# Kernel tuning notes

Hardware: AMD Instinct MI355X
Metric: run time of the kernel (lower is better)

The kernel has to match this reference:

```python
import jax, jax.numpy as jnp
import numpy as np

EMB = 1024
HEADS = 16
HEAD_DIM = EMB // HEADS


def setup_inputs() -> dict:
    key = jax.random.key(0)
    ks = jax.random.split(key, 5)
    x = jax.random.normal(ks[0], (2, 2048, EMB), dtype=jnp.float32)
    # per-head projection params, stacked over heads: [H, E, D]
    Wq = jax.random.normal(ks[1], (HEADS, EMB, HEAD_DIM), dtype=jnp.float32)
    Wk = jax.random.normal(ks[2], (HEADS, EMB, HEAD_DIM), dtype=jnp.float32)
    Wv = jax.random.normal(ks[3], (HEADS, EMB, HEAD_DIM), dtype=jnp.float32)
    # output projection (torch Linear weight [out, in], bias=False)
    Wo = jax.random.normal(ks[4], (EMB, EMB), dtype=jnp.float32) * (1.0 / np.sqrt(EMB))
    return {"x": x, "Wq": Wq, "Wk": Wk, "Wv": Wv, "Wo": Wo}


def reference(x, Wq, Wk, Wv, Wo):
    B, T, E = x.shape
    # per-head projections: [B, H, T, D]
    q = jnp.einsum('bte,hed->bhtd', x, Wq)
    k = jnp.einsum('bte,hed->bhtd', x, Wk)
    v = jnp.einsum('bte,hed->bhtd', x, Wv)
    scale = 1.0 / jnp.sqrt(jnp.asarray(HEAD_DIM, dtype=x.dtype))
    scores = jnp.einsum('bhtd,bhsd->bhts', q, k) * scale  # [B,H,T,T]
    s = jax.nn.softmax(scores, axis=-1)
    out = jnp.einsum('bhts,bhsd->bhtd', s, v)
    # concat heads along last dim in head order: [B, T, H*D]
    combined = jnp.transpose(out, (0, 2, 1, 3)).reshape(B, T, E)
    # residual + output projection (Linear bias=False: y = combined @ Wo.T)
    return x + combined @ Wo.T
```

## Files before the change

kernel.cpp:

```cpp
#include <hip/hip_runtime.h>

#define EMB   1024
#define HEADS 16
#define HDIM  64
#define BATCH 2
#define SEQ   2048
#define MROWS (BATCH*SEQ)
#define STR   40
#define QSCALE 0.1803368801111204f

typedef __attribute__((ext_vector_type(8))) short bf16x8;
typedef __attribute__((ext_vector_type(4))) float f32x4;
typedef unsigned short u16;

__device__ __forceinline__ u16 f2bf(float f) {
    unsigned u = __float_as_uint(f);
    u += 0x7fffu + ((u >> 16) & 1u);
    return (u16)(u >> 16);
}
__device__ __forceinline__ float bf2f(u16 h) {
    return __uint_as_float((unsigned)h << 16);
}
__device__ __forceinline__ float fast_exp2(float x) {
#if __has_builtin(__builtin_amdgcn_exp2f)
    return __builtin_amdgcn_exp2f(x);
#else
    return __expf(x * 0.6931471805599453f);
#endif
}
__device__ __forceinline__ unsigned pk_trunc(float lo, float hi) {
    return __builtin_amdgcn_perm(__float_as_uint(hi), __float_as_uint(lo),
                                 0x07060302u);
}

#define SWZ(r, ch) ((((r) << 6)) + ((((ch) ^ ((r) & 7))) << 3))

__global__ __launch_bounds__(256)
void prep1(const float* __restrict__ X, const float* __restrict__ Wq,
           const float* __restrict__ Wk,
           u16* __restrict__ Xh, u16* __restrict__ Xl,
           u16* __restrict__ Qth, u16* __restrict__ Qtl,
           u16* __restrict__ Kth, u16* __restrict__ Ktl)
{
    const int bx = blockIdx.x;
    if (bx < 2048) {
        int i = (bx * 256 + threadIdx.x) * 8;
#pragma unroll
        for (int half = 0; half < 2; ++half) {
            float4 v = *(const float4*)(X + i + half * 4);
            ushort4 hi, lo;
            hi.x = f2bf(v.x); lo.x = f2bf(v.x - bf2f(hi.x));
            hi.y = f2bf(v.y); lo.y = f2bf(v.y - bf2f(hi.y));
            hi.z = f2bf(v.z); lo.z = f2bf(v.z - bf2f(hi.z));
            hi.w = f2bf(v.w); lo.w = f2bf(v.w - bf2f(hi.w));
            *(ushort4*)(Xh + i + half * 4) = hi;
            *(ushort4*)(Xl + i + half * 4) = lo;
        }
    } else {
        const int f = bx - 2048;
        const int z = f >> 9, y = (f >> 5) & 15, x = f & 31;
        const float* W  = z ? Wk  : Wq;
        u16* Oh         = z ? Kth : Qth;
        u16* Ol         = z ? Ktl : Qtl;
        const int d  = threadIdx.x & 63;
        const int e0 = (x * 4 + (threadIdx.x >> 6)) * 8;
        const float* src = W + ((size_t)y * EMB + e0) * HDIM + d;
        ushort4 h0, h1, l0, l1;
        float v; u16 hv;
        v = src[0 * 64]; hv = f2bf(v); h0.x = hv; l0.x = f2bf(v - bf2f(hv));
        v = src[1 * 64]; hv = f2bf(v); h0.y = hv; l0.y = f2bf(v - bf2f(hv));
        v = src[2 * 64]; hv = f2bf(v); h0.z = hv; l0.z = f2bf(v - bf2f(hv));
        v = src[3 * 64]; hv = f2bf(v); h0.w = hv; l0.w = f2bf(v - bf2f(hv));
        v = src[4 * 64]; hv = f2bf(v); h1.x = hv; l1.x = f2bf(v - bf2f(hv));
        v = src[5 * 64]; hv = f2bf(v); h1.y = hv; l1.y = f2bf(v - bf2f(hv));
        v = src[6 * 64]; hv = f2bf(v); h1.z = hv; l1.z = f2bf(v - bf2f(hv));
        v = src[7 * 64]; hv = f2bf(v); h1.w = hv; l1.w = f2bf(v - bf2f(hv));
        size_t obase = ((size_t)y * HDIM + d) * EMB + e0;
        *(ushort4*)(Oh + obase)     = h0;
        *(ushort4*)(Oh + obase + 4) = h1;
        *(ushort4*)(Ol + obase)     = l0;
        *(ushort4*)(Ol + obase + 4) = l1;
    }
}

__global__ __launch_bounds__(256)
void prep2(const float* __restrict__ Wv, const float* __restrict__ Wo,
           u16* __restrict__ Vth, u16* __restrict__ Woh)
{
    const int f = blockIdx.x;
    if (f < 512) {
        const int y = f >> 5, x = f & 31;
        const int d  = threadIdx.x & 63;
        const int e0 = (x * 4 + (threadIdx.x >> 6)) * 8;
        const float* src = Wv + ((size_t)y * EMB + e0) * HDIM + d;
        ushort4 h0, h1;
        h0.x = f2bf(src[0 * 64]); h0.y = f2bf(src[1 * 64]);
        h0.z = f2bf(src[2 * 64]); h0.w = f2bf(src[3 * 64]);
        h1.x = f2bf(src[4 * 64]); h1.y = f2bf(src[5 * 64]);
        h1.z = f2bf(src[6 * 64]); h1.w = f2bf(src[7 * 64]);
        size_t obase = ((size_t)y * HDIM + d) * EMB + e0;
        *(ushort4*)(Vth + obase)     = h0;
        *(ushort4*)(Vth + obase + 4) = h1;
    } else {
        int i = ((f - 512) * 256 + threadIdx.x) * 8;
#pragma unroll
        for (int half = 0; half < 2; ++half) {
            float4 v = *(const float4*)(Wo + i + half * 4);
            ushort4 o;
            o.x = f2bf(v.x); o.y = f2bf(v.y); o.z = f2bf(v.z); o.w = f2bf(v.w);
            *(ushort4*)(Woh + i + half * 4) = o;
        }
    }
}

__global__ __launch_bounds__(256, 2)
void qkv_z01(const u16* __restrict__ Xh, const u16* __restrict__ Xl,
             const u16* __restrict__ Wqh, const u16* __restrict__ Wql,
             const u16* __restrict__ Wkh, const u16* __restrict__ Wkl,
             u16* __restrict__ Qh, u16* __restrict__ Ql,
             u16* __restrict__ Kh, u16* __restrict__ Kl)
{
    const int z  = blockIdx.z;
    const int m0 = blockIdx.x * 128;
    const int n0 = blockIdx.y * 128;
    const int t    = threadIdx.x;
    const int wave = t >> 6, lane = t & 63;
    const int wm = wave & 1, wn = wave >> 1;
    const int l16 = lane & 15, quad = lane >> 4;

    __shared__ u16 Ahs[128][STR];
    __shared__ u16 Als[128][STR];
    __shared__ u16 Bhs[128][STR];
    __shared__ u16 Bls[128][STR];

    const u16* Bh_g = z ? Wkh : Wqh;
    const u16* Bl_g = z ? Wkl : Wql;

    const int ar0 = t >> 2, ak = (t & 3) * 8, ar1 = ar0 + 64;

    f32x4 acc[4][4];
#pragma unroll
    for (int i = 0; i < 4; ++i)
#pragma unroll
        for (int j = 0; j < 4; ++j) acc[i][j] = (f32x4){0.f, 0.f, 0.f, 0.f};

    bf16x8 cur[8], nxt[8], nx2[8];
#define QK_LOAD(dst, kk)                                                        \
    do {                                                                        \
        dst[0] = *(const bf16x8*)(Xh  + (size_t)(m0 + ar0) * EMB + (kk) + ak);  \
        dst[1] = *(const bf16x8*)(Xh  + (size_t)(m0 + ar1) * EMB + (kk) + ak);  \
        dst[2] = *(const bf16x8*)(Xl  + (size_t)(m0 + ar0) * EMB + (kk) + ak);  \
        dst[3] = *(const bf16x8*)(Xl  + (size_t)(m0 + ar1) * EMB + (kk) + ak);  \
        dst[4] = *(const bf16x8*)(Bh_g + (size_t)(n0 + ar0) * EMB + (kk) + ak); \
        dst[5] = *(const bf16x8*)(Bh_g + (size_t)(n0 + ar1) * EMB + (kk) + ak); \
        dst[6] = *(const bf16x8*)(Bl_g + (size_t)(n0 + ar0) * EMB + (kk) + ak); \
        dst[7] = *(const bf16x8*)(Bl_g + (size_t)(n0 + ar1) * EMB + (kk) + ak); \
    } while (0)

    QK_LOAD(cur, 0);
    QK_LOAD(nxt, 32);

    for (int k0 = 0; k0 < EMB; k0 += 32) {
        __syncthreads();
        *(bf16x8*)&Ahs[ar0][ak] = cur[0];  *(bf16x8*)&Ahs[ar1][ak] = cur[1];
        *(bf16x8*)&Als[ar0][ak] = cur[2];  *(bf16x8*)&Als[ar1][ak] = cur[3];
        *(bf16x8*)&Bhs[ar0][ak] = cur[4];  *(bf16x8*)&Bhs[ar1][ak] = cur[5];
        *(bf16x8*)&Bls[ar0][ak] = cur[6];  *(bf16x8*)&Bls[ar1][ak] = cur[7];
        __syncthreads();

        const int kn = (k0 + 64 < EMB) ? k0 + 64 : 0;
        QK_LOAD(nx2, kn);

        bf16x8 B4h[4], B4l[4];
#pragma unroll
        for (int j = 0; j < 4; ++j) {
            B4h[j] = *(const bf16x8*)&Bhs[wn * 64 + 16 * j + l16][quad * 8];
            B4l[j] = *(const bf16x8*)&Bls[wn * 64 + 16 * j + l16][quad * 8];
        }
#pragma unroll
        for (int i = 0; i < 4; ++i) {
            bf16x8 Ai_h = *(const bf16x8*)&Ahs[wm * 64 + 16 * i + l16][quad * 8];
            bf16x8 Ai_l = *(const bf16x8*)&Als[wm * 64 + 16 * i + l16][quad * 8];
#pragma unroll
            for (int j = 0; j < 4; ++j) {
                acc[i][j] = __builtin_amdgcn_mfma_f32_16x16x32_bf16(Ai_h, B4h[j], acc[i][j], 0, 0, 0);
                acc[i][j] = __builtin_amdgcn_mfma_f32_16x16x32_bf16(Ai_h, B4l[j], acc[i][j], 0, 0, 0);
                acc[i][j] = __builtin_amdgcn_mfma_f32_16x16x32_bf16(Ai_l, B4h[j], acc[i][j], 0, 0, 0);
            }
        }
#pragma unroll
        for (int q = 0; q < 8; ++q) { cur[q] = nxt[q]; nxt[q] = nx2[q]; }
    }
#undef QK_LOAD

    const int b = m0 >> 11;
    const int h = (n0 + wn * 64) >> 6;
    u16* Oh = z ? Kh : Qh;
    u16* Ol = z ? Kl : Ql;
    const float esc = z ? 1.0f : QSCALE;
#pragma unroll
    for (int i = 0; i < 4; ++i)
#pragma unroll
        for (int r = 0; r < 4; ++r) {
            int tt = (m0 & (SEQ - 1)) + wm * 64 + 16 * i + quad * 4 + r;
            size_t rowbase = ((size_t)(b * HEADS + h) * SEQ + tt) * HDIM;
#pragma unroll
            for (int j = 0; j < 4; ++j) {
                int d = 16 * j + l16;
                float v = acc[i][j][r] * esc;
                u16 hv = f2bf(v);
                Oh[rowbase + d] = hv;
                Ol[rowbase + d] = f2bf(v - bf2f(hv));
            }
        }
}

__global__ __launch_bounds__(256, 2)
void qkv_v(const u16* __restrict__ Xh, const u16* __restrict__ Wvt,
           u16* __restrict__ Vt)
{
    const int m0 = blockIdx.x * 128;
    const int n0 = blockIdx.y * 128;
    const int t    = threadIdx.x;
    const int wave = t >> 6, lane = t & 63;
    const int wm = wave & 1, wn = wave >> 1;
    const int l16 = lane & 15, quad = lane >> 4;

    __shared__ u16 Ahs[128][STR];
    __shared__ u16 Bhs[128][STR];

    const int ar0 = t >> 2, ak = (t & 3) * 8, ar1 = ar0 + 64;

    f32x4 acc[4][4];
#pragma unroll
    for (int i = 0; i < 4; ++i)
#pragma unroll
        for (int j = 0; j < 4; ++j) acc[i][j] = (f32x4){0.f, 0.f, 0.f, 0.f};

    bf16x8 cur[4], nxt[4], nx2[4];
#define V_LOAD(dst, kk)                                                         \
    do {                                                                        \
        dst[0] = *(const bf16x8*)(Xh  + (size_t)(m0 + ar0) * EMB + (kk) + ak);  \
        dst[1] = *(const bf16x8*)(Xh  + (size_t)(m0 + ar1) * EMB + (kk) + ak);  \
        dst[2] = *(const bf16x8*)(Wvt + (size_t)(n0 + ar0) * EMB + (kk) + ak);  \
        dst[3] = *(const bf16x8*)(Wvt + (size_t)(n0 + ar1) * EMB + (kk) + ak);  \
    } while (0)

    V_LOAD(cur, 0);
    V_LOAD(nxt, 32);

    for (int k0 = 0; k0 < EMB; k0 += 32) {
        __syncthreads();
        *(bf16x8*)&Ahs[ar0][ak] = cur[0];  *(bf16x8*)&Ahs[ar1][ak] = cur[1];
        *(bf16x8*)&Bhs[ar0][ak] = cur[2];  *(bf16x8*)&Bhs[ar1][ak] = cur[3];
        __syncthreads();

        const int kn = (k0 + 64 < EMB) ? k0 + 64 : 0;
        V_LOAD(nx2, kn);

        bf16x8 B4[4];
#pragma unroll
        for (int j = 0; j < 4; ++j)
            B4[j] = *(const bf16x8*)&Bhs[wn * 64 + 16 * j + l16][quad * 8];
#pragma unroll
        for (int i = 0; i < 4; ++i) {
            bf16x8 Ai = *(const bf16x8*)&Ahs[wm * 64 + 16 * i + l16][quad * 8];
#pragma unroll
            for (int j = 0; j < 4; ++j)
                acc[i][j] = __builtin_amdgcn_mfma_f32_16x16x32_bf16(Ai, B4[j], acc[i][j], 0, 0, 0);
        }
#pragma unroll
        for (int q = 0; q < 4; ++q) { cur[q] = nxt[q]; nxt[q] = nx2[q]; }
    }
#undef V_LOAD

    const int b = m0 >> 11;
    const int h = (n0 + wn * 64) >> 6;
#pragma unroll
    for (int i = 0; i < 4; ++i)
#pragma unroll
        for (int j = 0; j < 4; ++j) {
            int d  = 16 * j + l16;
            int tt = (m0 & (SEQ - 1)) + wm * 64 + 16 * i + quad * 4;
            ushort4 o;
            o.x = f2bf(acc[i][j][0]); o.y = f2bf(acc[i][j][1]);
            o.z = f2bf(acc[i][j][2]); o.w = f2bf(acc[i][j][3]);
            *(ushort4*)(Vt + ((size_t)(b * HEADS + h) * HDIM + d) * SEQ + tt) = o;
        }
}

__global__ __launch_bounds__(256, 2)
void attn_mfma(const u16* __restrict__ Qh, const u16* __restrict__ Ql,
               const u16* __restrict__ Kh, const u16* __restrict__ Kl,
               const u16* __restrict__ Vt, u16* __restrict__ Cb)
{
    const int qt0  = blockIdx.x * 128;
    const int bh   = blockIdx.y;
    const int t    = threadIdx.x;
    const int wave = t >> 6;
    const int lane = t & 63;
    const int l16  = lane & 15;
    const int quad = lane >> 4;

    __shared__ u16 Ksh[4096];
    __shared__ u16 Ksl[4096];
    __shared__ u16 Vs [4096];
    __shared__ u16 Ps [8192];

    const size_t bh_off = (size_t)bh * SEQ * HDIM;
    const u16* Qhb = Qh + bh_off;
    const u16* Qlb = Ql + bh_off;
    const u16* Khb = Kh + bh_off;
    const u16* Klb = Kl + bh_off;
    const u16* Vtb = Vt + bh_off;

    bf16x8 aQh[2][2], aQl[2][2];
#pragma unroll
    for (int g = 0; g < 2; ++g) {
        const int qrow = qt0 + g * 64 + wave * 16 + l16;
        const u16* bH = Qhb + (size_t)qrow * HDIM + quad * 8;
        const u16* bL = Qlb + (size_t)qrow * HDIM + quad * 8;
        aQh[g][0] = *(const bf16x8*)(bH);
        aQh[g][1] = *(const bf16x8*)(bH + 32);
        aQl[g][0] = *(const bf16x8*)(bL);
        aQl[g][1] = *(const bf16x8*)(bL + 32);
    }

    f32x4 accO[2][4];
    float m_i[2] = {-1e30f, -1e30f}, l_i[2] = {0.f, 0.f};
#pragma unroll
    for (int g = 0; g < 2; ++g)
#pragma unroll
        for (int j = 0; j < 4; ++j) accO[g][j] = (f32x4){0.f, 0.f, 0.f, 0.f};

    const int sr0 = t >> 3, sch = t & 7, sr1 = sr0 + 32;
    const int gc  = sch * 8;
    const int so0 = SWZ(sr0, sch), so1 = SWZ(sr1, sch);

    bf16x8 cur[6], nxt[6];
#define KV_LOAD(dst, ss)                                                       \
    do {                                                                       \
        dst[0] = *(const bf16x8*)(Khb + (size_t)((ss) + sr0) * HDIM + gc);     \
        dst[1] = *(const bf16x8*)(Khb + (size_t)((ss) + sr1) * HDIM + gc);     \
        dst[2] = *(const bf16x8*)(Klb + (size_t)((ss) + sr0) * HDIM + gc);     \
        dst[3] = *(const bf16x8*)(Klb + (size_t)((ss) + sr1) * HDIM + gc);     \
        dst[4] = *(const bf16x8*)(Vtb + (size_t)sr0 * SEQ + (ss) + gc);        \
        dst[5] = *(const bf16x8*)(Vtb + (size_t)sr1 * SEQ + (ss) + gc);        \
    } while (0)

    KV_LOAD(cur, 0);

    for (int s0 = 0; s0 < SEQ; s0 += 64) {
        __syncthreads();
        *(bf16x8*)&Ksh[so0] = cur[0];  *(bf16x8*)&Ksh[so1] = cur[1];
        *(bf16x8*)&Ksl[so0] = cur[2];  *(bf16x8*)&Ksl[so1] = cur[3];
        *(bf16x8*)&Vs [so0] = cur[4];  *(bf16x8*)&Vs [so1] = cur[5];
        __syncthreads();

        const int sn = (s0 + 64 < SEQ) ? s0 + 64 : 0;
        KV_LOAD(nxt, sn);

        f32x4 accS[2][4];
#pragma unroll
        for (int g = 0; g < 2; ++g)
#pragma unroll
            for (int i = 0; i < 4; ++i) accS[g][i] = (f32x4){0.f, 0.f, 0.f, 0.f};
#pragma unroll
        for (int c = 0; c < 2; ++c) {
#pragma unroll
            for (int i = 0; i < 4; ++i) {
                bf16x8 kh_ = *(const bf16x8*)&Ksh[SWZ(16 * i + l16, 4 * c + quad)];
                bf16x8 kl_ = *(const bf16x8*)&Ksl[SWZ(16 * i + l16, 4 * c + quad)];
                accS[0][i] = __builtin_amdgcn_mfma_f32_16x16x32_bf16(kh_, aQh[0][c], accS[0][i], 0, 0, 0);
                accS[0][i] = __builtin_amdgcn_mfma_f32_16x16x32_bf16(kl_, aQh[0][c], accS[0][i], 0, 0, 0);
                accS[0][i] = __builtin_amdgcn_mfma_f32_16x16x32_bf16(kh_, aQl[0][c], accS[0][i], 0, 0, 0);
                accS[1][i] = __builtin_amdgcn_mfma_f32_16x16x32_bf16(kh_, aQh[1][c], accS[1][i], 0, 0, 0);
                accS[1][i] = __builtin_amdgcn_mfma_f32_16x16x32_bf16(kl_, aQh[1][c], accS[1][i], 0, 0, 0);
                accS[1][i] = __builtin_amdgcn_mfma_f32_16x16x32_bf16(kh_, aQl[1][c], accS[1][i], 0, 0, 0);
            }
        }

#pragma unroll
        for (int g = 0; g < 2; ++g) {
            float vmax = fmaxf(fmaxf(accS[g][0][0], accS[g][0][1]),
                               fmaxf(accS[g][0][2], accS[g][0][3]));
#pragma unroll
            for (int i = 1; i < 4; ++i)
                vmax = fmaxf(vmax, fmaxf(fmaxf(accS[g][i][0], accS[g][i][1]),
                                         fmaxf(accS[g][i][2], accS[g][i][3])));
            vmax = fmaxf(vmax, __shfl_xor(vmax, 16, 64));
            vmax = fmaxf(vmax, __shfl_xor(vmax, 32, 64));
            float mn   = fmaxf(m_i[g], vmax);
            float alph = fast_exp2(m_i[g] - mn);
            m_i[g] = mn;
            float P[4][4], s = 0.f;
#pragma unroll
            for (int i = 0; i < 4; ++i)
#pragma unroll
                for (int r = 0; r < 4; ++r) {
                    P[i][r] = fast_exp2(accS[g][i][r] - mn);
                    s += P[i][r];
                }
            s += __shfl_xor(s, 16, 64);
            s += __shfl_xor(s, 32, 64);
            l_i[g] = l_i[g] * alph + s;
#pragma unroll
            for (int j = 0; j < 4; ++j) accO[g][j] *= alph;

            const int prow = g * 64 + wave * 16 + l16;
#pragma unroll
            for (int i = 0; i < 4; ++i) {
                uint2 pv;
                pv.x = pk_trunc(P[i][0], P[i][1]);
                pv.y = pk_trunc(P[i][2], P[i][3]);
                *(uint2*)&Ps[SWZ(prow, 2 * i + (quad >> 1)) + ((quad & 1) << 2)] = pv;
            }
        }

#pragma unroll
        for (int c = 0; c < 2; ++c) {
            bf16x8 bP0 = *(const bf16x8*)&Ps[SWZ(wave * 16 + l16,      4 * c + quad)];
            bf16x8 bP1 = *(const bf16x8*)&Ps[SWZ(64 + wave * 16 + l16, 4 * c + quad)];
#pragma unroll
            for (int j = 0; j < 4; ++j) {
                bf16x8 aV = *(const bf16x8*)&Vs[SWZ(16 * j + l16, 4 * c + quad)];
                accO[0][j] = __builtin_amdgcn_mfma_f32_16x16x32_bf16(aV, bP0, accO[0][j], 0, 0, 0);
                accO[1][j] = __builtin_amdgcn_mfma_f32_16x16x32_bf16(aV, bP1, accO[1][j], 0, 0, 0);
            }
        }
#pragma unroll
        for (int q = 0; q < 6; ++q) cur[q] = nxt[q];
    }
#undef KV_LOAD

    const int b = bh >> 4, h = bh & 15;
#pragma unroll
    for (int g = 0; g < 2; ++g) {
        const int row = qt0 + g * 64 + wave * 16 + l16;
        const float inv = 1.f / l_i[g];
#pragma unroll
        for (int j = 0; j < 4; ++j) {
            ushort4 o;
            o.x = f2bf(accO[g][j][0] * inv); o.y = f2bf(accO[g][j][1] * inv);
            o.z = f2bf(accO[g][j][2] * inv); o.w = f2bf(accO[g][j][3] * inv);
            *(ushort4*)&Cb[((size_t)b * SEQ + row) * EMB + h * HDIM + 16 * j + quad * 4] = o;
        }
    }
}

__global__ __launch_bounds__(256, 2)
void oproj_mfma(const u16* __restrict__ Cb, const u16* __restrict__ Woh,
                const float* __restrict__ X, float* __restrict__ Y)
{
    const int m0 = blockIdx.x * 128;
    const int n0 = blockIdx.y * 128;
    const int t    = threadIdx.x;
    const int wave = t >> 6, lane = t & 63;
    const int wm = wave & 1, wn = wave >> 1;
    const int l16 = lane & 15, quad = lane >> 4;

    __shared__ u16 Ahs[128][STR];
    __shared__ u16 Bhs[128][STR];

    const int ar0 = t >> 2, ak = (t & 3) * 8, ar1 = ar0 + 64;

    f32x4 acc[4][4];
#pragma unroll
    for (int i = 0; i < 4; ++i)
#pragma unroll
        for (int j = 0; j < 4; ++j) acc[i][j] = (f32x4){0.f, 0.f, 0.f, 0.f};

    bf16x8 cur[4], nxt[4], nx2[4];
#define O_LOAD(dst, kk)                                                         \
    do {                                                                        \
        dst[0] = *(const bf16x8*)(Cb  + (size_t)(m0 + ar0) * EMB + (kk) + ak);  \
        dst[1] = *(const bf16x8*)(Cb  + (size_t)(m0 + ar1) * EMB + (kk) + ak);  \
        dst[2] = *(const bf16x8*)(Woh + (size_t)(n0 + ar0) * EMB + (kk) + ak);  \
        dst[3] = *(const bf16x8*)(Woh + (size_t)(n0 + ar1) * EMB + (kk) + ak);  \
    } while (0)

    O_LOAD(cur, 0);
    O_LOAD(nxt, 32);

    for (int k0 = 0; k0 < EMB; k0 += 32) {
        __syncthreads();
        *(bf16x8*)&Ahs[ar0][ak] = cur[0];  *(bf16x8*)&Ahs[ar1][ak] = cur[1];
        *(bf16x8*)&Bhs[ar0][ak] = cur[2];  *(bf16x8*)&Bhs[ar1][ak] = cur[3];
        __syncthreads();

        const int kn = (k0 + 64 < EMB) ? k0 + 64 : 0;
        O_LOAD(nx2, kn);

        bf16x8 B4[4];
#pragma unroll
        for (int j = 0; j < 4; ++j)
            B4[j] = *(const bf16x8*)&Bhs[wn * 64 + 16 * j + l16][quad * 8];
#pragma unroll
        for (int i = 0; i < 4; ++i) {
            bf16x8 Ai = *(const bf16x8*)&Ahs[wm * 64 + 16 * i + l16][quad * 8];
#pragma unroll
            for (int j = 0; j < 4; ++j)
                acc[i][j] = __builtin_amdgcn_mfma_f32_16x16x32_bf16(Ai, B4[j], acc[i][j], 0, 0, 0);
        }
#pragma unroll
        for (int q = 0; q < 4; ++q) { cur[q] = nxt[q]; nxt[q] = nx2[q]; }
    }
#undef O_LOAD

#pragma unroll
    for (int i = 0; i < 4; ++i)
#pragma unroll
        for (int r = 0; r < 4; ++r) {
            int m = m0 + wm * 64 + 16 * i + quad * 4 + r;
#pragma unroll
            for (int j = 0; j < 4; ++j) {
                int n = n0 + wn * 64 + 16 * j + l16;
                Y[(size_t)m * EMB + n] = acc[i][j][r] + X[(size_t)m * EMB + n];
            }
        }
}

extern "C" void kernel_launch(void* const* d_in, const int* in_sizes, int n_in,
                              void* d_out, int out_size, void* d_ws,
                              size_t ws_size, hipStream_t stream)
{
    const float* x  = (const float*)d_in[0];
    const float* Wq = (const float*)d_in[1];
    const float* Wk = (const float*)d_in[2];
    const float* Wv = (const float*)d_in[3];
    const float* Wo = (const float*)d_in[4];
    float* Y = (float*)d_out;

    const size_t NPER = (size_t)MROWS * EMB;
    u16* base  = (u16*)d_ws;
    u16* Qh    = base;
    u16* Ql    = Qh + NPER;
    u16* Kh    = Ql + NPER;
    u16* Kl    = Kh + NPER;
    u16* Vt    = Kl + NPER;
    u16* Xh    = Vt + NPER;
    u16* Xl    = Xh + NPER;
    u16* Wtq_h = Xl + NPER;
    u16* Wtq_l = Wtq_h + EMB * EMB;
    u16* Wtk_h = Wtq_l + EMB * EMB;
    u16* Wtk_l = Wtk_h + EMB * EMB;
    u16* Wvt   = Wtq_h;
    u16* Cb    = Xh;
    u16* Woh   = Xl;

    prep1<<<dim3(3072), 256, 0, stream>>>(x, Wq, Wk, Xh, Xl,
                                          Wtq_h, Wtq_l, Wtk_h, Wtk_l);
    qkv_z01<<<dim3(32, 8, 2), 256, 0, stream>>>(Xh, Xl, Wtq_h, Wtq_l,
                                                Wtk_h, Wtk_l, Qh, Ql, Kh, Kl);
    prep2<<<dim3(1024), 256, 0, stream>>>(Wv, Wo, Wvt, Woh);
    qkv_v<<<dim3(32, 8), 256, 0, stream>>>(Xh, Wvt, Vt);
    attn_mfma<<<dim3(SEQ / 128, BATCH * HEADS), 256, 0, stream>>>(Qh, Ql, Kh, Kl,
                                                                  Vt, Cb);
    oproj_mfma<<<dim3(32, 8), 256, 0, stream>>>(Cb, Woh, x, Y);
}
```

Before: 266.4 us.

## Load MFMA operands directly from global memory, dropping LDS staging

Result: slower. 468.7 us (+75.9%).

```diff
diff --git a/kernel.cpp b/kernel.cpp
--- a/kernel.cpp
+++ b/kernel.cpp
@@ -6,7 +6,6 @@
 #define BATCH 2
 #define SEQ   2048
 #define MROWS (BATCH*SEQ)
-#define STR   40
 #define QSCALE 0.1803368801111204f
 
 typedef __attribute__((ext_vector_type(8))) short bf16x8;
@@ -128,15 +127,17 @@
     const int wm = wave & 1, wn = wave >> 1;
     const int l16 = lane & 15, quad = lane >> 4;
 
-    __shared__ u16 Ahs[128][STR];
-    __shared__ u16 Als[128][STR];
-    __shared__ u16 Bhs[128][STR];
-    __shared__ u16 Bls[128][STR];
-
     const u16* Bh_g = z ? Wkh : Wqh;
     const u16* Bl_g = z ? Wkl : Wql;
 
-    const int ar0 = t >> 2, ak = (t & 3) * 8, ar1 = ar0 + 64;
+    const u16* Arow[4];  const u16* Brow[4];
+#pragma unroll
+    for (int i = 0; i < 4; ++i) {
+        Arow[i] = Xh   + (size_t)(m0 + wm * 64 + 16 * i + l16) * EMB + quad * 8;
+        Brow[i] = Bh_g + (size_t)(n0 + wn * 64 + 16 * i + l16) * EMB + quad * 8;
+    }
+    const ptrdiff_t dlo_a = Xl - Xh;
+    const ptrdiff_t dlo_b = Bl_g - Bh_g;
 
     f32x4 acc[4][4];
 #pragma unroll
@@ -144,52 +145,34 @@
 #pragma unroll
         for (int j = 0; j < 4; ++j) acc[i][j] = (f32x4){0.f, 0.f, 0.f, 0.f};
 
-    bf16x8 cur[8], nxt[8], nx2[8];
-#define QK_LOAD(dst, kk)                                                        \
-    do {                                                                        \
-        dst[0] = *(const bf16x8*)(Xh  + (size_t)(m0 + ar0) * EMB + (kk) + ak);  \
-        dst[1] = *(const bf16x8*)(Xh  + (size_t)(m0 + ar1) * EMB + (kk) + ak);  \
-        dst[2] = *(const bf16x8*)(Xl  + (size_t)(m0 + ar0) * EMB + (kk) + ak);  \
-        dst[3] = *(const bf16x8*)(Xl  + (size_t)(m0 + ar1) * EMB + (kk) + ak);  \
-        dst[4] = *(const bf16x8*)(Bh_g + (size_t)(n0 + ar0) * EMB + (kk) + ak); \
-        dst[5] = *(const bf16x8*)(Bh_g + (size_t)(n0 + ar1) * EMB + (kk) + ak); \
-        dst[6] = *(const bf16x8*)(Bl_g + (size_t)(n0 + ar0) * EMB + (kk) + ak); \
-        dst[7] = *(const bf16x8*)(Bl_g + (size_t)(n0 + ar1) * EMB + (kk) + ak); \
+    bf16x8 Ah[4], Al[4], Bh[4], Bl[4], nAh[4], nAl[4], nBh[4], nBl[4];
+#define QK_LOAD(ah, al, bhh, bll, kk)                                          \
+    do {                                                                       \
+        _Pragma("unroll") for (int i = 0; i < 4; ++i) {                        \
+            ah[i]  = *(const bf16x8*)(Arow[i] + (kk));                         \
+            al[i]  = *(const bf16x8*)(Arow[i] + dlo_a + (kk));                 \
+            bhh[i] = *(const bf16x8*)(Brow[i] + (kk));                         \
+            bll[i] = *(const bf16x8*)(Brow[i] + dlo_b + (kk));                 \
+        }                                                                      \
     } while (0)
 
-    QK_LOAD(cur, 0);
-    QK_LOAD(nxt, 32);
+    QK_LOAD(Ah, Al, Bh, Bl, 0);
 
     for (int k0 = 0; k0 < EMB; k0 += 32) {
-        __syncthreads();
-        *(bf16x8*)&Ahs[ar0][ak] = cur[0];  *(bf16x8*)&Ahs[ar1][ak] = cur[1];
-        *(bf16x8*)&Als[ar0][ak] = cur[2];  *(bf16x8*)&Als[ar1][ak] = cur[3];
-        *(bf16x8*)&Bhs[ar0][ak] = cur[4];  *(bf16x8*)&Bhs[ar1][ak] = cur[5];
-        *(bf16x8*)&Bls[ar0][ak] = cur[6];  *(bf16x8*)&Bls[ar1][ak] = cur[7];
-        __syncthreads();
-
-        const int kn = (k0 + 64 < EMB) ? k0 + 64 : 0;
-        QK_LOAD(nx2, kn);
-
-        bf16x8 B4h[4], B4l[4];
-#pragma unroll
-        for (int j = 0; j < 4; ++j) {
-            B4h[j] = *(const bf16x8*)&Bhs[wn * 64 + 16 * j + l16][quad * 8];
-            B4l[j] = *(const bf16x8*)&Bls[wn * 64 + 16 * j + l16][quad * 8];
-        }
-#pragma unroll
-        for (int i = 0; i < 4; ++i) {
-            bf16x8 Ai_h = *(const bf16x8*)&Ahs[wm * 64 + 16 * i + l16][quad * 8];
-            bf16x8 Ai_l = *(const bf16x8*)&Als[wm * 64 + 16 * i + l16][quad * 8];
+        const int kn = (k0 + 32 < EMB) ? k0 + 32 : 0;
+        QK_LOAD(nAh, nAl, nBh, nBl, kn);
+#pragma unroll
+        for (int i = 0; i < 4; ++i)
 #pragma unroll
             for (int j = 0; j < 4; ++j) {
-                acc[i][j] = __builtin_amdgcn_mfma_f32_16x16x32_bf16(Ai_h, B4h[j], acc[i][j], 0, 0, 0);
-                acc[i][j] = __builtin_amdgcn_mfma_f32_16x16x32_bf16(Ai_h, B4l[j], acc[i][j], 0, 0, 0);
-                acc[i][j] = __builtin_amdgcn_mfma_f32_16x16x32_bf16(Ai_l, B4h[j], acc[i][j], 0, 0, 0);
-            }
-        }
-#pragma unroll
-        for (int q = 0; q < 8; ++q) { cur[q] = nxt[q]; nxt[q] = nx2[q]; }
+                acc[i][j] = __builtin_amdgcn_mfma_f32_16x16x32_bf16(Ah[i], Bh[j], acc[i][j], 0, 0, 0);
+                acc[i][j] = __builtin_amdgcn_mfma_f32_16x16x32_bf16(Ah[i], Bl[j], acc[i][j], 0, 0, 0);
+                acc[i][j] = __builtin_amdgcn_mfma_f32_16x16x32_bf16(Al[i], Bh[j], acc[i][j], 0, 0, 0);
+            }
+#pragma unroll
+        for (int q = 0; q < 4; ++q) {
+            Ah[q] = nAh[q]; Al[q] = nAl[q]; Bh[q] = nBh[q]; Bl[q] = nBl[q];
+        }
     }
 #undef QK_LOAD
 
@@ -226,10 +209,12 @@
     const int wm = wave & 1, wn = wave >> 1;
     const int l16 = lane & 15, quad = lane >> 4;
 
-    __shared__ u16 Ahs[128][STR];
-    __shared__ u16 Bhs[128][STR];
-
-    const int ar0 = t >> 2, ak = (t & 3) * 8, ar1 = ar0 + 64;
+    const u16* Arow[4];  const u16* Brow[4];
+#pragma unroll
+    for (int i = 0; i < 4; ++i) {
+        Arow[i] = Xh  + (size_t)(m0 + wm * 64 + 16 * i + l16) * EMB + quad * 8;
+        Brow[i] = Wvt + (size_t)(n0 + wn * 64 + 16 * i + l16) * EMB + quad * 8;
+    }
 
     f32x4 acc[4][4];
 #pragma unroll
@@ -237,42 +222,28 @@
 #pragma unroll
         for (int j = 0; j < 4; ++j) acc[i][j] = (f32x4){0.f, 0.f, 0.f, 0.f};
 
-    bf16x8 cur[4], nxt[4], nx2[4];
-#define V_LOAD(dst, kk)                                                         \
-    do {                                                                        \
-        dst[0] = *(const bf16x8*)(Xh  + (size_t)(m0 + ar0) * EMB + (kk) + ak);  \
-        dst[1] = *(const bf16x8*)(Xh  + (size_t)(m0 + ar1) * EMB + (kk) + ak);  \
-        dst[2] = *(const bf16x8*)(Wvt + (size_t)(n0 + ar0) * EMB + (kk) + ak);  \
-        dst[3] = *(const bf16x8*)(Wvt + (size_t)(n0 + ar1) * EMB + (kk) + ak);  \
-    } while (0)
-
-    V_LOAD(cur, 0);
-    V_LOAD(nxt, 32);
+    bf16x8 A[4], B[4], nA[4], nB[4];
+#pragma unroll
+    for (int i = 0; i < 4; ++i) {
+        A[i] = *(const bf16x8*)(Arow[i]);
+        B[i] = *(const bf16x8*)(Brow[i]);
+    }
 
     for (int k0 = 0; k0 < EMB; k0 += 32) {
-        __syncthreads();
-        *(bf16x8*)&Ahs[ar0][ak] = cur[0];  *(bf16x8*)&Ahs[ar1][ak] = cur[1];
-        *(bf16x8*)&Bhs[ar0][ak] = cur[2];  *(bf16x8*)&Bhs[ar1][ak] = cur[3];
-        __syncthreads();
-
-        const int kn = (k0 + 64 < EMB) ? k0 + 64 : 0;
-        V_LOAD(nx2, kn);
-
-        bf16x8 B4[4];
-#pragma unroll
-        for (int j = 0; j < 4; ++j)
-            B4[j] = *(const bf16x8*)&Bhs[wn * 64 + 16 * j + l16][quad * 8];
+        const int kn = (k0 + 32 < EMB) ? k0 + 32 : 0;
 #pragma unroll
         for (int i = 0; i < 4; ++i) {
-            bf16x8 Ai = *(const bf16x8*)&Ahs[wm * 64 + 16 * i + l16][quad * 8];
+            nA[i] = *(const bf16x8*)(Arow[i] + kn);
+            nB[i] = *(const bf16x8*)(Brow[i] + kn);
+        }
+#pragma unroll
+        for (int i = 0; i < 4; ++i)
 #pragma unroll
             for (int j = 0; j < 4; ++j)
-                acc[i][j] = __builtin_amdgcn_mfma_f32_16x16x32_bf16(Ai, B4[j], acc[i][j], 0, 0, 0);
-        }
-#pragma unroll
-        for (int q = 0; q < 4; ++q) { cur[q] = nxt[q]; nxt[q] = nx2[q]; }
-    }
-#undef V_LOAD
+                acc[i][j] = __builtin_amdgcn_mfma_f32_16x16x32_bf16(A[i], B[j], acc[i][j], 0, 0, 0);
+#pragma unroll
+        for (int q = 0; q < 4; ++q) { A[q] = nA[q]; B[q] = nB[q]; }
+    }
 
     const int b = m0 >> 11;
     const int h = (n0 + wn * 64) >> 6;
@@ -302,10 +273,7 @@
     const int l16  = lane & 15;
     const int quad = lane >> 4;
 
-    __shared__ u16 Ksh[4096];
-    __shared__ u16 Ksl[4096];
-    __shared__ u16 Vs [4096];
-    __shared__ u16 Ps [8192];
+    __shared__ u16 Ps[8192];
 
     const size_t bh_off = (size_t)bh * SEQ * HDIM;
     const u16* Qhb = Qh + bh_off;
@@ -326,6 +294,14 @@
         aQl[g][1] = *(const bf16x8*)(bL + 32);
     }
 
+    const u16* Krow[4];  const u16* Vrow[4];
+#pragma unroll
+    for (int i = 0; i < 4; ++i) {
+        Krow[i] = Khb + (size_t)(16 * i + l16) * HDIM + quad * 8;
+        Vrow[i] = Vtb + (size_t)(16 * i + l16) * SEQ  + quad * 8;
+    }
+    const ptrdiff_t dlo_k = Klb - Khb;
+
     f32x4 accO[2][4];
     float m_i[2] = {-1e30f, -1e30f}, l_i[2] = {0.f, 0.f};
 #pragma unroll
@@ -333,32 +309,16 @@
 #pragma unroll
         for (int j = 0; j < 4; ++j) accO[g][j] = (f32x4){0.f, 0.f, 0.f, 0.f};
 
-    const int sr0 = t >> 3, sch = t & 7, sr1 = sr0 + 32;
-    const int gc  = sch * 8;
-    const int so0 = SWZ(sr0, sch), so1 = SWZ(sr1, sch);
-
-    bf16x8 cur[6], nxt[6];
-#define KV_LOAD(dst, ss)                                                       \
-    do {                                                                       \
-        dst[0] = *(const bf16x8*)(Khb + (size_t)((ss) + sr0) * HDIM + gc);     \
-        dst[1] = *(const bf16x8*)(Khb + (size_t)((ss) + sr1) * HDIM + gc);     \
-        dst[2] = *(const bf16x8*)(Klb + (size_t)((ss) + sr0) * HDIM + gc);     \
-        dst[3] = *(const bf16x8*)(Klb + (size_t)((ss) + sr1) * HDIM + gc);     \
-        dst[4] = *(const bf16x8*)(Vtb + (size_t)sr0 * SEQ + (ss) + gc);        \
-        dst[5] = *(const bf16x8*)(Vtb + (size_t)sr1 * SEQ + (ss) + gc);        \
-    } while (0)
-
-    KV_LOAD(cur, 0);
-
     for (int s0 = 0; s0 < SEQ; s0 += 64) {
-        __syncthreads();
-        *(bf16x8*)&Ksh[so0] = cur[0];  *(bf16x8*)&Ksh[so1] = cur[1];
-        *(bf16x8*)&Ksl[so0] = cur[2];  *(bf16x8*)&Ksl[so1] = cur[3];
-        *(bf16x8*)&Vs [so0] = cur[4];  *(bf16x8*)&Vs [so1] = cur[5];
-        __syncthreads();
-
-        const int sn = (s0 + 64 < SEQ) ? s0 + 64 : 0;
-        KV_LOAD(nxt, sn);
+        bf16x8 kh[2][4], kl[2][4], vv[2][4];
+#pragma unroll
+        for (int c = 0; c < 2; ++c)
+#pragma unroll
+            for (int i = 0; i < 4; ++i) {
+                kh[c][i] = *(const bf16x8*)(Krow[i] + (size_t)s0 * HDIM + 32 * c);
+                kl[c][i] = *(const bf16x8*)(Krow[i] + dlo_k + (size_t)s0 * HDIM + 32 * c);
+                vv[c][i] = *(const bf16x8*)(Vrow[i] + s0 + 32 * c);
+            }
 
         f32x4 accS[2][4];
 #pragma unroll
@@ -369,14 +329,12 @@
         for (int c = 0; c < 2; ++c) {
 #pragma unroll
             for (int i = 0; i < 4; ++i) {
-                bf16x8 kh_ = *(const bf16x8*)&Ksh[SWZ(16 * i + l16, 4 * c + quad)];
-                bf16x8 kl_ = *(const bf16x8*)&Ksl[SWZ(16 * i + l16, 4 * c + quad)];
-                accS[0][i] = __builtin_amdgcn_mfma_f32_16x16x32_bf16(kh_, aQh[0][c], accS[0][i], 0, 0, 0);
-                accS[0][i] = __builtin_amdgcn_mfma_f32_16x16x32_bf16(kl_, aQh[0][c], accS[0][i], 0, 0, 0);
-                accS[0][i] = __builtin_amdgcn_mfma_f32_16x16x32_bf16(kh_, aQl[0][c], accS[0][i], 0, 0, 0);
-                accS[1][i] = __builtin_amdgcn_mfma_f32_16x16x32_bf16(kh_, aQh[1][c], accS[1][i], 0, 0, 0);
-                accS[1][i] = __builtin_amdgcn_mfma_f32_16x16x32_bf16(kl_, aQh[1][c], accS[1][i], 0, 0, 0);
-                accS[1][i] = __builtin_amdgcn_mfma_f32_16x16x32_bf16(kh_, aQl[1][c], accS[1][i], 0, 0, 0);
+                accS[0][i] = __builtin_amdgcn_mfma_f32_16x16x32_bf16(kh[c][i], aQh[0][c], accS[0][i], 0, 0, 0);
+                accS[0][i] = __builtin_amdgcn_mfma_f32_16x16x32_bf16(kl[c][i], aQh[0][c], accS[0][i], 0, 0, 0);
+                accS[0][i] = __builtin_amdgcn_mfma_f32_16x16x32_bf16(kh[c][i], aQl[0][c], accS[0][i], 0, 0, 0);
+                accS[1][i] = __builtin_amdgcn_mfma_f32_16x16x32_bf16(kh[c][i], aQh[1][c], accS[1][i], 0, 0, 0);
+                accS[1][i] = __builtin_amdgcn_mfma_f32_16x16x32_bf16(kl[c][i], aQh[1][c], accS[1][i], 0, 0, 0);
+                accS[1][i] = __builtin_amdgcn_mfma_f32_16x16x32_bf16(kh[c][i], aQl[1][c], accS[1][i], 0, 0, 0);
             }
         }
 
@@ -423,15 +381,11 @@
             bf16x8 bP1 = *(const bf16x8*)&Ps[SWZ(64 + wave * 16 + l16, 4 * c + quad)];
 #pragma unroll
             for (int j = 0; j < 4; ++j) {
-                bf16x8 aV = *(const bf16x8*)&Vs[SWZ(16 * j + l16, 4 * c + quad)];
-                accO[0][j] = __builtin_amdgcn_mfma_f32_16x16x32_bf16(aV, bP0, accO[0][j], 0, 0, 0);
-                accO[1][j] = __builtin_amdgcn_mfma_f32_16x16x32_bf16(aV, bP1, accO[1][j], 0, 0, 0);
-            }
-        }
-#pragma unroll
-        for (int q = 0; q < 6; ++q) cur[q] = nxt[q];
-    }
-#undef KV_LOAD
+                accO[0][j] = __builtin_amdgcn_mfma_f32_16x16x32_bf16(vv[c][j], bP0, accO[0][j], 0, 0, 0);
+                accO[1][j] = __builtin_amdgcn_mfma_f32_16x16x32_bf16(vv[c][j], bP1, accO[1][j], 0, 0, 0);
+            }
+        }
+    }
 
     const int b = bh >> 4, h = bh & 15;
 #pragma unroll
@@ -459,10 +413,12 @@
     const int wm = wave & 1, wn = wave >> 1;
     const int l16 = lane & 15, quad = lane >> 4;
 
-    __shared__ u16 Ahs[128][STR];
-    __shared__ u16 Bhs[128][STR];
-
-    const int ar0 = t >> 2, ak = (t & 3) * 8, ar1 = ar0 + 64;
+    const u16* Arow[4];  const u16* Brow[4];
+#pragma unroll
+    for (int i = 0; i < 4; ++i) {
+        Arow[i] = Cb  + (size_t)(m0 + wm * 64 + 16 * i + l16) * EMB + quad * 8;
+        Brow[i] = Woh + (size_t)(n0 + wn * 64 + 16 * i + l16) * EMB + quad * 8;
+    }
 
     f32x4 acc[4][4];
 #pragma unroll
@@ -470,42 +426,28 @@
 #pragma unroll
         for (int j = 0; j < 4; ++j) acc[i][j] = (f32x4){0.f, 0.f, 0.f, 0.f};
 
-    bf16x8 cur[4], nxt[4], nx2[4];
-#define O_LOAD(dst, kk)                                                         \
-    do {                                                                        \
-        dst[0] = *(const bf16x8*)(Cb  + (size_t)(m0 + ar0) * EMB + (kk) + ak);  \
-        dst[1] = *(const bf16x8*)(Cb  + (size_t)(m0 + ar1) * EMB + (kk) + ak);  \
-        dst[2] = *(const bf16x8*)(Woh + (size_t)(n0 + ar0) * EMB + (kk) + ak);  \
-        dst[3] = *(const bf16x8*)(Woh + (size_t)(n0 + ar1) * EMB + (kk) + ak);  \
-    } while (0)
-
-    O_LOAD(cur, 0);
-    O_LOAD(nxt, 32);
+    bf16x8 A[4], B[4], nA[4], nB[4];
+#pragma unroll
+    for (int i = 0; i < 4; ++i) {
+        A[i] = *(const bf16x8*)(Arow[i]);
+        B[i] = *(const bf16x8*)(Brow[i]);
+    }
 
     for (int k0 = 0; k0 < EMB; k0 += 32) {
-        __syncthreads();
-        *(bf16x8*)&Ahs[ar0][ak] = cur[0];  *(bf16x8*)&Ahs[ar1][ak] = cur[1];
-        *(bf16x8*)&Bhs[ar0][ak] = cur[2];  *(bf16x8*)&Bhs[ar1][ak] = cur[3];
-        __syncthreads();
-
-        const int kn = (k0 + 64 < EMB) ? k0 + 64 : 0;
-        O_LOAD(nx2, kn);
-
-        bf16x8 B4[4];
-#pragma unroll
-        for (int j = 0; j < 4; ++j)
-            B4[j] = *(const bf16x8*)&Bhs[wn * 64 + 16 * j + l16][quad * 8];
+        const int kn = (k0 + 32 < EMB) ? k0 + 32 : 0;
 #pragma unroll
         for (int i = 0; i < 4; ++i) {
-            bf16x8 Ai = *(const bf16x8*)&Ahs[wm * 64 + 16 * i + l16][quad * 8];
+            nA[i] = *(const bf16x8*)(Arow[i] + kn);
+            nB[i] = *(const bf16x8*)(Brow[i] + kn);
+        }
+#pragma unroll
+        for (int i = 0; i < 4; ++i)
 #pragma unroll
             for (int j = 0; j < 4; ++j)
-                acc[i][j] = __builtin_amdgcn_mfma_f32_16x16x32_bf16(Ai, B4[j], acc[i][j], 0, 0, 0);
-        }
-#pragma unroll
-        for (int q = 0; q < 4; ++q) { cur[q] = nxt[q]; nxt[q] = nx2[q]; }
-    }
-#undef O_LOAD
+                acc[i][j] = __builtin_amdgcn_mfma_f32_16x16x32_bf16(A[i], B[j], acc[i][j], 0, 0, 0);
+#pragma unroll
+        for (int q = 0; q < 4; ++q) { A[q] = nA[q]; B[q] = nB[q]; }
+    }
 
 #pragma unroll
     for (int i = 0; i < 4; ++i)
```

## Double-buffer LDS tiles in GEMM and attention kernels to drop a barrier

Applied to the files above, without the earlier changes.

After: 269.1 us. Within noise of the previous version (+1.0%).

```diff
diff --git a/kernel.cpp b/kernel.cpp
--- a/kernel.cpp
+++ b/kernel.cpp
@@ -226,8 +226,8 @@
     const int wm = wave & 1, wn = wave >> 1;
     const int l16 = lane & 15, quad = lane >> 4;
 
-    __shared__ u16 Ahs[128][STR];
-    __shared__ u16 Bhs[128][STR];
+    __shared__ u16 Ahs[2][128][STR];
+    __shared__ u16 Bhs[2][128][STR];
 
     const int ar0 = t >> 2, ak = (t & 3) * 8, ar1 = ar0 + 64;
 
@@ -237,7 +237,7 @@
 #pragma unroll
         for (int j = 0; j < 4; ++j) acc[i][j] = (f32x4){0.f, 0.f, 0.f, 0.f};
 
-    bf16x8 cur[4], nxt[4], nx2[4];
+    bf16x8 cur[4];
 #define V_LOAD(dst, kk)                                                         \
     do {                                                                        \
         dst[0] = *(const bf16x8*)(Xh  + (size_t)(m0 + ar0) * EMB + (kk) + ak);  \
@@ -247,30 +247,30 @@
     } while (0)
 
     V_LOAD(cur, 0);
-    V_LOAD(nxt, 32);
+    *(bf16x8*)&Ahs[0][ar0][ak] = cur[0];  *(bf16x8*)&Ahs[0][ar1][ak] = cur[1];
+    *(bf16x8*)&Bhs[0][ar0][ak] = cur[2];  *(bf16x8*)&Bhs[0][ar1][ak] = cur[3];
 
     for (int k0 = 0; k0 < EMB; k0 += 32) {
+        const int buf = (k0 >> 5) & 1;
         __syncthreads();
-        *(bf16x8*)&Ahs[ar0][ak] = cur[0];  *(bf16x8*)&Ahs[ar1][ak] = cur[1];
-        *(bf16x8*)&Bhs[ar0][ak] = cur[2];  *(bf16x8*)&Bhs[ar1][ak] = cur[3];
-        __syncthreads();
-
-        const int kn = (k0 + 64 < EMB) ? k0 + 64 : 0;
-        V_LOAD(nx2, kn);
+        const int kn = (k0 + 32 < EMB) ? k0 + 32 : 0;
+        V_LOAD(cur, kn);
 
         bf16x8 B4[4];
 #pragma unroll
         for (int j = 0; j < 4; ++j)
-            B4[j] = *(const bf16x8*)&Bhs[wn * 64 + 16 * j + l16][quad * 8];
+            B4[j] = *(const bf16x8*)&Bhs[buf][wn * 64 + 16 * j + l16][quad * 8];
 #pragma unroll
         for (int i = 0; i < 4; ++i) {
-            bf16x8 Ai = *(const bf16x8*)&Ahs[wm * 64 + 16 * i + l16][quad * 8];
+            bf16x8 Ai = *(const bf16x8*)&Ahs[buf][wm * 64 + 16 * i + l16][quad * 8];
 #pragma unroll
             for (int j = 0; j < 4; ++j)
                 acc[i][j] = __builtin_amdgcn_mfma_f32_16x16x32_bf16(Ai, B4[j], acc[i][j], 0, 0, 0);
         }
-#pragma unroll
-        for (int q = 0; q < 4; ++q) { cur[q] = nxt[q]; nxt[q] = nx2[q]; }
+        *(bf16x8*)&Ahs[buf ^ 1][ar0][ak] = cur[0];
+        *(bf16x8*)&Ahs[buf ^ 1][ar1][ak] = cur[1];
+        *(bf16x8*)&Bhs[buf ^ 1][ar0][ak] = cur[2];
+        *(bf16x8*)&Bhs[buf ^ 1][ar1][ak] = cur[3];
     }
 #undef V_LOAD
 
@@ -302,9 +302,9 @@
     const int l16  = lane & 15;
     const int quad = lane >> 4;
 
-    __shared__ u16 Ksh[4096];
-    __shared__ u16 Ksl[4096];
-    __shared__ u16 Vs [4096];
+    __shared__ u16 Ksh[2][4096];
+    __shared__ u16 Ksl[2][4096];
+    __shared__ u16 Vs [2][4096];
     __shared__ u16 Ps [8192];
 
     const size_t bh_off = (size_t)bh * SEQ * HDIM;
@@ -337,7 +337,7 @@
     const int gc  = sch * 8;
     const int so0 = SWZ(sr0, sch), so1 = SWZ(sr1, sch);
 
-    bf16x8 cur[6], nxt[6];
+    bf16x8 cur[6];
 #define KV_LOAD(dst, ss)                                                       \
     do {                                                                       \
         dst[0] = *(const bf16x8*)(Khb + (size_t)((ss) + sr0) * HDIM + gc);     \
@@ -349,16 +349,15 @@
     } while (0)
 
     KV_LOAD(cur, 0);
+    *(bf16x8*)&Ksh[0][so0] = cur[0];  *(bf16x8*)&Ksh[0][so1] = cur[1];
+    *(bf16x8*)&Ksl[0][so0] = cur[2];  *(bf16x8*)&Ksl[0][so1] = cur[3];
+    *(bf16x8*)&Vs [0][so0] = cur[4];  *(bf16x8*)&Vs [0][so1] = cur[5];
 
     for (int s0 = 0; s0 < SEQ; s0 += 64) {
+        const int buf = (s0 >> 6) & 1;
         __syncthreads();
-        *(bf16x8*)&Ksh[so0] = cur[0];  *(bf16x8*)&Ksh[so1] = cur[1];
-        *(bf16x8*)&Ksl[so0] = cur[2];  *(bf16x8*)&Ksl[so1] = cur[3];
-        *(bf16x8*)&Vs [so0] = cur[4];  *(bf16x8*)&Vs [so1] = cur[5];
-        __syncthreads();
-
         const int sn = (s0 + 64 < SEQ) ? s0 + 64 : 0;
-        KV_LOAD(nxt, sn);
+        KV_LOAD(cur, sn);
 
         f32x4 accS[2][4];
 #pragma unroll
@@ -369,8 +368,8 @@
         for (int c = 0; c < 2; ++c) {
 #pragma unroll
             for (int i = 0; i < 4; ++i) {
-                bf16x8 kh_ = *(const bf16x8*)&Ksh[SWZ(16 * i + l16, 4 * c + quad)];
-                bf16x8 kl_ = *(const bf16x8*)&Ksl[SWZ(16 * i + l16, 4 * c + quad)];
+                bf16x8 kh_ = *(const bf16x8*)&Ksh[buf][SWZ(16 * i + l16, 4 * c + quad)];
+                bf16x8 kl_ = *(const bf16x8*)&Ksl[buf][SWZ(16 * i + l16, 4 * c + quad)];
                 accS[0][i] = __builtin_amdgcn_mfma_f32_16x16x32_bf16(kh_, aQh[0][c], accS[0][i], 0, 0, 0);
                 accS[0][i] = __builtin_amdgcn_mfma_f32_16x16x32_bf16(kl_, aQh[0][c], accS[0][i], 0, 0, 0);
                 accS[0][i] = __builtin_amdgcn_mfma_f32_16x16x32_bf16(kh_, aQl[0][c], accS[0][i], 0, 0, 0);
@@ -423,13 +422,15 @@
             bf16x8 bP1 = *(const bf16x8*)&Ps[SWZ(64 + wave * 16 + l16, 4 * c + quad)];
 #pragma unroll
             for (int j = 0; j < 4; ++j) {
-                bf16x8 aV = *(const bf16x8*)&Vs[SWZ(16 * j + l16, 4 * c + quad)];
+                bf16x8 aV = *(const bf16x8*)&Vs[buf][SWZ(16 * j + l16, 4 * c + quad)];
                 accO[0][j] = __builtin_amdgcn_mfma_f32_16x16x32_bf16(aV, bP0, accO[0][j], 0, 0, 0);
                 accO[1][j] = __builtin_amdgcn_mfma_f32_16x16x32_bf16(aV, bP1, accO[1][j], 0, 0, 0);
             }
         }
-#pragma unroll
-        for (int q = 0; q < 6; ++q) cur[q] = nxt[q];
+
+        *(bf16x8*)&Ksh[buf ^ 1][so0] = cur[0];  *(bf16x8*)&Ksh[buf ^ 1][so1] = cur[1];
+        *(bf16x8*)&Ksl[buf ^ 1][so0] = cur[2];  *(bf16x8*)&Ksl[buf ^ 1][so1] = cur[3];
+        *(bf16x8*)&Vs [buf ^ 1][so0] = cur[4];  *(bf16x8*)&Vs [buf ^ 1][so1] = cur[5];
     }
 #undef KV_LOAD
 
@@ -459,8 +460,8 @@
     const int wm = wave & 1, wn = wave >> 1;
     const int l16 = lane & 15, quad = lane >> 4;
 
-    __shared__ u16 Ahs[128][STR];
-    __shared__ u16 Bhs[128][STR];
+    __shared__ u16 Ahs[2][128][STR];
+    __shared__ u16 Bhs[2][128][STR];
 
     const int ar0 = t >> 2, ak = (t & 3) * 8, ar1 = ar0 + 64;
 
@@ -470,7 +471,7 @@
 #pragma unroll
         for (int j = 0; j < 4; ++j) acc[i][j] = (f32x4){0.f, 0.f, 0.f, 0.f};
 
-    bf16x8 cur[4], nxt[4], nx2[4];
+    bf16x8 cur[4];
 #define O_LOAD(dst, kk)                                                         \
     do {                                                                        \
         dst[0] = *(const bf16x8*)(Cb  + (size_t)(m0 + ar0) * EMB + (kk) + ak);  \
@@ -480,30 +481,30 @@
     } while (0)
 
     O_LOAD(cur, 0);
-    O_LOAD(nxt, 32);
+    *(bf16x8*)&Ahs[0][ar0][ak] = cur[0];  *(bf16x8*)&Ahs[0][ar1][ak] = cur[1];
+    *(bf16x8*)&Bhs[0][ar0][ak] = cur[2];  *(bf16x8*)&Bhs[0][ar1][ak] = cur[3];
 
     for (int k0 = 0; k0 < EMB; k0 += 32) {
+        const int buf = (k0 >> 5) & 1;
         __syncthreads();
-        *(bf16x8*)&Ahs[ar0][ak] = cur[0];  *(bf16x8*)&Ahs[ar1][ak] = cur[1];
-        *(bf16x8*)&Bhs[ar0][ak] = cur[2];  *(bf16x8*)&Bhs[ar1][ak] = cur[3];
-        __syncthreads();
-
-        const int kn = (k0 + 64 < EMB) ? k0 + 64 : 0;
-        O_LOAD(nx2, kn);
+        const int kn = (k0 + 32 < EMB) ? k0 + 32 : 0;
+        O_LOAD(cur, kn);
 
         bf16x8 B4[4];
 #pragma unroll
         for (int j = 0; j < 4; ++j)
-            B4[j] = *(const bf16x8*)&Bhs[wn * 64 + 16 * j + l16][quad * 8];
+            B4[j] = *(const bf16x8*)&Bhs[buf][wn * 64 + 16 * j + l16][quad * 8];
 #pragma unroll
         for (int i = 0; i < 4; ++i) {
-            bf16x8 Ai = *(const bf16x8*)&Ahs[wm * 64 + 16 * i + l16][quad * 8];
+            bf16x8 Ai = *(const bf16x8*)&Ahs[buf][wm * 64 + 16 * i + l16][quad * 8];
 #pragma unroll
             for (int j = 0; j < 4; ++j)
                 acc[i][j] = __builtin_amdgcn_mfma_f32_16x16x32_bf16(Ai, B4[j], acc[i][j], 0, 0, 0);
         }
-#pragma unroll
-        for (int q = 0; q < 4; ++q) { cur[q] = nxt[q]; nxt[q] = nx2[q]; }
+        *(bf16x8*)&Ahs[buf ^ 1][ar0][ak] = cur[0];
+        *(bf16x8*)&Ahs[buf ^ 1][ar1][ak] = cur[1];
+        *(bf16x8*)&Bhs[buf ^ 1][ar0][ak] = cur[2];
+        *(bf16x8*)&Bhs[buf ^ 1][ar1][ak] = cur[3];
     }
 #undef O_LOAD
 
```
